# Kernel tuning notes

Measured on AMD Instinct MI355X. Metric: run time of the kernel, lower is better.

Reference implementation:

```python
import jax, jax.numpy as jnp
import numpy as np

B, T, DI, D = 8, 256, 64, 128
PRED_LEN, OUT_DIM = 96, 7
LN_EPS = 1e-5


def setup_inputs() -> dict:
    key = jax.random.key(0)
    ks = jax.random.split(key, 10)
    s = lambda k, shape, sc: (jax.random.normal(k, shape, jnp.float32) * sc)
    return {
        'x': s(ks[0], (B, T, DI), 1.0),
        'W_b': s(ks[1], (DI, D), DI ** -0.5), 'b_b': jnp.zeros((D,), jnp.float32),
        'Wk': s(ks[2], (D, D), D ** -0.5),
        'Wv': s(ks[3], (D, D), D ** -0.5),
        'Wq': s(ks[4], (D, D), D ** -0.5),
        'W_m': s(ks[5], (D, 3), D ** -0.5), 'b_m': jnp.zeros((3,), jnp.float32),
        'W_f': s(ks[6], (2 * D, D), (2 * D) ** -0.5), 'b_f': jnp.zeros((D,), jnp.float32),
        'W1': s(ks[7], (D, D), D ** -0.5), 'b1': jnp.zeros((D,), jnp.float32),
        'g1': jnp.ones((D,), jnp.float32), 'be1': jnp.zeros((D,), jnp.float32),
        'W2': s(ks[8], (D, PRED_LEN * OUT_DIM), D ** -0.5),
        'b2': jnp.zeros((PRED_LEN * OUT_DIM,), jnp.float32),
    }


def _layernorm(h, g, b):
    mu = h.mean(-1, keepdims=True)
    var = jnp.mean((h - mu) ** 2, -1, keepdims=True)
    return (h - mu) * jax.lax.rsqrt(var + LN_EPS) * g + b


def _forward(x, W_b, b_b, Wk, Wv, Wq, W_m, b_m, W_f, b_f, W1, b1, g1, be1, W2, b2):
    # Backbone P: feature extraction -> f_t  [B,T,D]
    f = jax.nn.gelu(x @ W_b + b_b)
    # Meta-learner: per-step (theta_t, eta_t, alpha_t)
    meta = jax.nn.sigmoid(f @ W_m + b_m)               # [B,T,3]
    theta = 0.01 * meta[..., 0]                         # learning rate
    eta = meta[..., 1]                                  # momentum
    alpha = 0.1 * meta[..., 2]                          # forget/decay
    # Key/value/query projections (precomputed; recurrence is in M,S only)
    k = f @ Wk; v = f @ Wv; q = f @ Wq                  # [B,T,D] each
    seq = (jnp.swapaxes(k, 0, 1), jnp.swapaxes(v, 0, 1), jnp.swapaxes(q, 0, 1),
           theta.T, eta.T, alpha.T)                     # time-major
    M0 = jnp.zeros((B, D, D), f.dtype)
    S0 = jnp.zeros((B, D, D), f.dtype)

    def step(carry, inp):
        M, S = carry
        kt, vt, qt, th, et, al = inp
        # grad of 0.5*||M k - v||^2 wrt M  (rank-1 outer product)
        err = jnp.einsum('bij,bj->bi', M, kt) - vt
        grad = jnp.einsum('bi,bj->bij', err, kt)
        S = et[:, None, None] * S - th[:, None, None] * grad
        M = (1.0 - al)[:, None, None] * M + S
        m_t = jnp.einsum('bij,bj->bi', M, qt)           # retrieve
        return (M, S), m_t

    (_, _), m_seq = jax.lax.scan(step, (M0, S0), seq)
    m = jnp.swapaxes(m_seq, 0, 1)                       # [B,T,D]
    # Gated fusion
    gate = jax.nn.sigmoid(jnp.concatenate([f, m], -1) @ W_f + b_f)
    fused = f * gate + m * (1.0 - gate)
    # Prediction head on last timestep (dropout=0 / eval)
    last = fused[:, -1, :]
    h = jax.nn.gelu(_layernorm(last @ W1 + b1, g1, be1))
    out = h @ W2 + b2
    return out.reshape(B, PRED_LEN, OUT_DIM)


def reference(x, W_b, b_b, Wk, Wv, Wq, W_m, b_m, W_f, b_f, W1, b1, g1, be1, W2, b2):
    return _forward(x, W_b, b_b, Wk, Wv, Wq, W_m, b_m, W_f, b_f, W1, b1, g1, be1, W2, b2)
```

## Files before the change

### kernel.cpp

```cpp
#include <hip/hip_runtime.h>
#include <hip/hip_bf16.h>

#define BB 8
#define TT 256
#define DIN 64
#define DD 128

__device__ __forceinline__ float gelu_tanh(float x) {
  float x3 = x * x * x;
  return 0.5f * x * (1.0f + tanhf(0.7978845608028654f * (x + 0.044715f * x3)));
}
__device__ __forceinline__ float sigmoidf(float x) {
  return 1.0f / (1.0f + __expf(-x));
}

template <typename T> __device__ __forceinline__ float getv(const void* p, int i);
template <> __device__ __forceinline__ float getv<float>(const void* p, int i) {
  return ((const float*)p)[i];
}
template <> __device__ __forceinline__ float getv<__hip_bfloat16>(const void* p, int i) {
  return __bfloat162float(((const __hip_bfloat16*)p)[i]);
}

template <int CTRL>
__device__ __forceinline__ float dpp_add(float x) {
  int s = __builtin_amdgcn_update_dpp(0, __float_as_int(x), CTRL, 0xF, 0xF, true);
  return x + __int_as_float(s);
}

__device__ __forceinline__ float rowsum16(float p) {
  p = dpp_add<0xB1>(p);
  p = dpp_add<0x4E>(p);
  p = dpp_add<0x124>(p);
  p = dpp_add<0x128>(p);
  return p;
}

__device__ __forceinline__ void gload_lds16(const void* g, void* l) {
  __builtin_amdgcn_global_load_lds(
      (const __attribute__((address_space(1))) void*)g,
      (__attribute__((address_space(3))) void*)l, 16, 0, 0);
}

__global__ void k0_detect(const void* x, int* flag) {
  __shared__ int cnt;
  if (threadIdx.x == 0) cnt = 0;
  __syncthreads();
  const unsigned short* u = (const unsigned short*)x;
  int good = 0;
  for (int idx = threadIdx.x; idx < 2048; idx += 256) {
    unsigned int bits = ((unsigned int)u[idx]) << 16;
    float f = __uint_as_float(bits);
    float a = fabsf(f);
    if (a == 0.0f || (a > 1e-4f && a < 100.0f)) good++;
  }
  atomicAdd(&cnt, good);
  __syncthreads();
  if (threadIdx.x == 0) *flag = (cnt >= 1536) ? 1 : 0;
}

template <typename T>
__device__ void k1_body(const void* x, const void* W_b, const void* b_b,
                        const void* Wk, const void* Wv, const void* Wq,
                        const void* W_m, const void* b_m,
                        float* kout, float* vout, float* scal4,
                        float* q_last, float* f_last) {
  const int row = blockIdx.x;
  const int b = row >> 8, t = row & 255;
  const int tid = threadIdx.x;
  __shared__ float xs[DIN];
  __shared__ float fs[DD];
  if (tid < DIN) xs[tid] = getv<T>(x, row * DIN + tid);
  __syncthreads();

  float acc = getv<T>(b_b, tid);
#pragma unroll 8
  for (int d = 0; d < DIN; ++d) acc += xs[d] * getv<T>(W_b, d * DD + tid);
  float f = gelu_tanh(acc);
  fs[tid] = f;
  __syncthreads();

  float ak = 0.0f, av = 0.0f;
#pragma unroll 8
  for (int c = 0; c < DD; ++c) {
    float fc = fs[c];
    ak += fc * getv<T>(Wk, c * DD + tid);
    av += fc * getv<T>(Wv, c * DD + tid);
  }
  kout[row * DD + tid] = ak;
  vout[row * DD + tid] = av;

  if (t == TT - 1) {
    float aq = 0.0f;
#pragma unroll 8
    for (int c = 0; c < DD; ++c) aq += fs[c] * getv<T>(Wq, c * DD + tid);
    q_last[b * DD + tid] = aq;
    f_last[b * DD + tid] = f;
  }
  if (tid < 4) {
    float val = 0.0f;
    if (tid < 3) {
      float a = getv<T>(b_m, tid);
      for (int c = 0; c < DD; ++c) a += fs[c] * getv<T>(W_m, c * 3 + tid);
      float s = sigmoidf(a);
      val = (tid == 0) ? 0.01f * s : ((tid == 1) ? s : 0.1f * s);
    }
    scal4[row * 4 + tid] = val;
  }
}

__global__ __launch_bounds__(128) void k1_kern(
    const void* x, const void* W_b, const void* b_b, const void* Wk,
    const void* Wv, const void* Wq, const void* W_m, const void* b_m,
    const int* flag, float* kout, float* vout, float* scal4, float* q_last,
    float* f_last) {
  if (*flag)
    k1_body<__hip_bfloat16>(x, W_b, b_b, Wk, Wv, Wq, W_m, b_m, kout, vout,
                            scal4, q_last, f_last);
  else
    k1_body<float>(x, W_b, b_b, Wk, Wv, Wq, W_m, b_m, kout, vout, scal4,
                   q_last, f_last);
}

__global__ __launch_bounds__(64) void k2_scan(
    const float* __restrict__ kbuf, const float* __restrict__ vbuf,
    const float* __restrict__ scal, const float* __restrict__ q_last,
    float* __restrict__ m_last) {
  const int tid = threadIdx.x;
  const int g = tid & 15;
  const int cidx = tid >> 4;
  const int chain = blockIdx.x * 4 + cidx;
  const int b = chain >> 7;
  const int i = chain & 127;
  const int i0 = (blockIdx.x * 4) & 127;

  __shared__ float kl[2][32 * DD];
  __shared__ float vl[TT * 4];
  __shared__ float4 scl[TT];

  const float* kslice = kbuf + (size_t)b * TT * DD;
  const float* vslice = vbuf + (size_t)b * TT * DD;

  for (int idx = tid; idx < TT * 4; idx += 64)
    vl[idx] = vslice[(idx >> 2) * DD + i0 + (idx & 3)];
  const float4* sp4 = (const float4*)scal + b * TT;
  for (int idx = tid; idx < TT; idx += 64) scl[idx] = sp4[idx];

#define K2_GLL(CH, BUF)                                                      \
  {                                                                          \
    const float* gs = kslice + (CH) * 32 * DD + tid * 4;                     \
    _Pragma("unroll") for (int j = 0; j < 16; ++j)                           \
        gload_lds16(gs + j * 256, &kl[BUF][j * 256]);                        \
  }
  K2_GLL(0, 0);

  float4 Ma = {0, 0, 0, 0}, Mb = {0, 0, 0, 0};
  float4 Sa = {0, 0, 0, 0}, Sb = {0, 0, 0, 0};

#define K2_STEP(KA, KB, VV, SC)                                              \
  {                                                                          \
    float p = (Ma.x * KA.x + Ma.y * KA.y) + (Ma.z * KA.z + Ma.w * KA.w) +    \
              (Mb.x * KB.x + Mb.y * KB.y) + (Mb.z * KB.z + Mb.w * KB.w);     \
    p = rowsum16(p);                                                         \
    const float err = p - VV;                                                \
    const float c = SC.x * err;                             \
    const float et = SC.y;                                          \
    const float am = 1.0f - SC.z;                             \
    Sa.x = et * Sa.x - c * KA.x;  Ma.x = am * Ma.x + Sa.x;                   \
    Sa.y = et * Sa.y - c * KA.y;  Ma.y = am * Ma.y + Sa.y;                   \
    Sa.z = et * Sa.z - c * KA.z;  Ma.z = am * Ma.z + Sa.z;                   \
    Sa.w = et * Sa.w - c * KA.w;  Ma.w = am * Ma.w + Sa.w;                   \
    Sb.x = et * Sb.x - c * KB.x;  Mb.x = am * Mb.x + Sb.x;                   \
    Sb.y = et * Sb.y - c * KB.y;  Mb.y = am * Mb.y + Sb.y;                   \
    Sb.z = et * Sb.z - c * KB.z;  Mb.z = am * Mb.z + Sb.z;                   \
    Sb.w = et * Sb.w - c * KB.w;  Mb.w = am * Mb.w + Sb.w;                   \
  }

  for (int ch = 0; ch < 8; ++ch) {
    asm volatile("s_waitcnt vmcnt(0) lgkmcnt(0)" ::: "memory");
    if (ch < 7) K2_GLL(ch + 1, (ch + 1) & 1);

    const float* kc = &kl[ch & 1][0];
    const int tbase = ch * 32;

    float4 ka = *(const float4*)(kc + g * 8);
    float4 kb = *(const float4*)(kc + g * 8 + 4);
    float vv = vl[tbase * 4 + cidx];
    float4 sc = scl[tbase];

#pragma unroll
    for (int tt = 0; tt < 32; ++tt) {
      float4 nka, nkb, nsc;
      float nv;
      if (tt < 31) {
        nka = *(const float4*)(kc + (tt + 1) * DD + g * 8);
        nkb = *(const float4*)(kc + (tt + 1) * DD + g * 8 + 4);
        nv = vl[(tbase + tt + 1) * 4 + cidx];
        nsc = scl[tbase + tt + 1];
      }
      K2_STEP(ka, kb, vv, sc);
      if (tt < 31) { ka = nka; kb = nkb; vv = nv; sc = nsc; }
    }
  }
#undef K2_STEP
#undef K2_GLL

  const float4* qp = (const float4*)(q_last + b * DD) + (g << 1);
  float4 qa = qp[0], qb = qp[1];
  float p = (Ma.x * qa.x + Ma.y * qa.y) + (Ma.z * qa.z + Ma.w * qa.w) +
            (Mb.x * qb.x + Mb.y * qb.y) + (Mb.z * qb.z + Mb.w * qb.w);
  p = rowsum16(p);
  if (g == 0) m_last[b * DD + i] = p;
}

template <typename T>
__device__ void k3_body(const float* f_last, const float* m_last,
                        const void* W_f, const void* b_f, const void* W1,
                        const void* b1, const void* g1, const void* be1,
                        const void* W2, const void* b2, void* out) {
  const int b = blockIdx.x, tid = threadIdx.x;
  __shared__ float fm[2 * DD];
  __shared__ float fused[DD];
  __shared__ float tmp[DD];
  __shared__ float h[DD];
  __shared__ float smu, srs;

  fm[tid] = (tid < DD) ? f_last[b * DD + tid] : m_last[b * DD + tid - DD];
  __syncthreads();

  if (tid < DD) {
    float a = getv<T>(b_f, tid);
#pragma unroll 8
    for (int c = 0; c < 2 * DD; ++c) a += fm[c] * getv<T>(W_f, c * DD + tid);
    float gte = sigmoidf(a);
    fused[tid] = fm[tid] * gte + fm[DD + tid] * (1.0f - gte);
  }
  __syncthreads();

  if (tid < DD) {
    float a = getv<T>(b1, tid);
#pragma unroll 8
    for (int c = 0; c < DD; ++c) a += fused[c] * getv<T>(W1, c * DD + tid);
    tmp[tid] = a;
  }
  __syncthreads();

  if (tid == 0) {
    float s = 0.0f;
    for (int c = 0; c < DD; ++c) s += tmp[c];
    float mu = s / (float)DD;
    float s2 = 0.0f;
    for (int c = 0; c < DD; ++c) {
      float d = tmp[c] - mu;
      s2 += d * d;
    }
    smu = mu;
    srs = rsqrtf(s2 / (float)DD + 1e-5f);
  }
  __syncthreads();

  if (tid < DD)
    h[tid] = gelu_tanh((tmp[tid] - smu) * srs * getv<T>(g1, tid) +
                       getv<T>(be1, tid));
  __syncthreads();

  for (int j = tid; j < 672; j += 256) {
    float a = getv<T>(b2, j);
#pragma unroll 8
    for (int c = 0; c < DD; ++c) a += h[c] * getv<T>(W2, c * 672 + j);
    if (sizeof(T) == 2)
      ((__hip_bfloat16*)out)[b * 672 + j] = __float2bfloat16(a);
    else
      ((float*)out)[b * 672 + j] = a;
  }
}

__global__ __launch_bounds__(256) void k3_kern(
    const float* f_last, const float* m_last, const void* W_f,
    const void* b_f, const void* W1, const void* b1, const void* g1,
    const void* be1, const void* W2, const void* b2, const int* flag,
    void* out) {
  if (*flag)
    k3_body<__hip_bfloat16>(f_last, m_last, W_f, b_f, W1, b1, g1, be1, W2, b2,
                            out);
  else
    k3_body<float>(f_last, m_last, W_f, b_f, W1, b1, g1, be1, W2, b2, out);
}

extern "C" void kernel_launch(void* const* d_in, const int* in_sizes, int n_in,
                              void* d_out, int out_size, void* d_ws,
                              size_t ws_size, hipStream_t stream) {
  const void* x   = d_in[0];
  const void* W_b = d_in[1];
  const void* b_b = d_in[2];
  const void* Wk  = d_in[3];
  const void* Wv  = d_in[4];
  const void* Wq  = d_in[5];
  const void* W_m = d_in[6];
  const void* b_m = d_in[7];
  const void* W_f = d_in[8];
  const void* b_f = d_in[9];
  const void* W1  = d_in[10];
  const void* b1  = d_in[11];
  const void* g1  = d_in[12];
  const void* be1 = d_in[13];
  const void* W2  = d_in[14];
  const void* b2  = d_in[15];

  float* w = (float*)d_ws;
  float* kbuf   = w;
  float* vbuf   = w + 262144;
  float* scal4  = w + 524288;
  float* q_last = w + 532480;
  float* f_last = w + 533504;
  float* m_last = w + 534528;
  int*   flag   = (int*)(w + 535552);

  k0_detect<<<1, 256, 0, stream>>>(x, flag);
  k1_kern<<<BB * TT, 128, 0, stream>>>(x, W_b, b_b, Wk, Wv, Wq, W_m, b_m,
                                       flag, kbuf, vbuf, scal4, q_last,
                                       f_last);
  k2_scan<<<256, 64, 0, stream>>>(kbuf, vbuf, scal4, q_last, m_last);
  k3_kern<<<BB, 256, 0, stream>>>(f_last, m_last, W_f, b_f, W1, b1, g1, be1,
                                  W2, b2, flag, d_out);
}
```

Measured before the change: 179.0 us.

## Split prediction head into two kernels with split-K parallel matvecs

The single 8-block head kernel is split in two. The first kernel uses 1024-thread blocks whose partial sums split the reduction dimension of the gate and W1 matvecs, and it computes LayerNorm statistics with wavefront shuffles instead of a serial loop in one thread. The second kernel spreads the W2 output matvec over 88 blocks, also splitting the reduction dimension. The aim is to shorten the serial tail after the scan, at the cost of one extra launch and a round-trip through global memory. Variance is now computed as E[x²]−μ², which is slightly less numerically robust.

```diff
diff --git a/kernel.cpp b/kernel.cpp
--- a/kernel.cpp
+++ b/kernel.cpp
@@ -214,77 +214,132 @@
 }
 
 template <typename T>
-__device__ void k3_body(const float* f_last, const float* m_last,
-                        const void* W_f, const void* b_f, const void* W1,
-                        const void* b1, const void* g1, const void* be1,
-                        const void* W2, const void* b2, void* out) {
+__device__ void k3a_body(const float* f_last, const float* m_last,
+                         const void* W_f, const void* b_f, const void* W1,
+                         const void* b1, const void* g1, const void* be1,
+                         float* h_buf) {
   const int b = blockIdx.x, tid = threadIdx.x;
+  const int o = tid & 127, s = tid >> 7;
   __shared__ float fm[2 * DD];
+  __shared__ float part[1024];
   __shared__ float fused[DD];
   __shared__ float tmp[DD];
-  __shared__ float h[DD];
   __shared__ float smu, srs;
 
-  fm[tid] = (tid < DD) ? f_last[b * DD + tid] : m_last[b * DD + tid - DD];
-  __syncthreads();
-
+  if (tid < 2 * DD)
+    fm[tid] = (tid < DD) ? f_last[b * DD + tid] : m_last[b * DD + tid - DD];
+  __syncthreads();
+
+  {
+    float a = 0.0f;
+#pragma unroll 8
+    for (int cc = 0; cc < 32; ++cc) {
+      const int c = s * 32 + cc;
+      a += fm[c] * getv<T>(W_f, c * DD + o);
+    }
+    part[tid] = a;
+  }
+  __syncthreads();
   if (tid < DD) {
     float a = getv<T>(b_f, tid);
-#pragma unroll 8
-    for (int c = 0; c < 2 * DD; ++c) a += fm[c] * getv<T>(W_f, c * DD + tid);
+#pragma unroll
+    for (int ss = 0; ss < 8; ++ss) a += part[ss * DD + tid];
     float gte = sigmoidf(a);
     fused[tid] = fm[tid] * gte + fm[DD + tid] * (1.0f - gte);
   }
   __syncthreads();
 
+  {
+    float a = 0.0f;
+#pragma unroll
+    for (int cc = 0; cc < 16; ++cc) {
+      const int c = s * 16 + cc;
+      a += fused[c] * getv<T>(W1, c * DD + o);
+    }
+    part[tid] = a;
+  }
+  __syncthreads();
   if (tid < DD) {
     float a = getv<T>(b1, tid);
-#pragma unroll 8
-    for (int c = 0; c < DD; ++c) a += fused[c] * getv<T>(W1, c * DD + tid);
+#pragma unroll
+    for (int ss = 0; ss < 8; ++ss) a += part[ss * DD + tid];
     tmp[tid] = a;
   }
   __syncthreads();
 
-  if (tid == 0) {
-    float s = 0.0f;
-    for (int c = 0; c < DD; ++c) s += tmp[c];
-    float mu = s / (float)DD;
-    float s2 = 0.0f;
-    for (int c = 0; c < DD; ++c) {
-      float d = tmp[c] - mu;
-      s2 += d * d;
-    }
-    smu = mu;
-    srs = rsqrtf(s2 / (float)DD + 1e-5f);
+  if (tid < 64) {
+    float x0 = tmp[tid], x1 = tmp[tid + 64];
+    float sm = x0 + x1;
+    float sq = x0 * x0 + x1 * x1;
+    sm = rowsum16(sm);
+    sq = rowsum16(sq);
+    sm += __shfl_xor(sm, 16); sq += __shfl_xor(sq, 16);
+    sm += __shfl_xor(sm, 32); sq += __shfl_xor(sq, 32);
+    if (tid == 0) {
+      float mu = sm / (float)DD;
+      smu = mu;
+      srs = rsqrtf(sq / (float)DD - mu * mu + 1e-5f);
+    }
   }
   __syncthreads();
 
   if (tid < DD)
-    h[tid] = gelu_tanh((tmp[tid] - smu) * srs * getv<T>(g1, tid) +
-                       getv<T>(be1, tid));
-  __syncthreads();
-
-  for (int j = tid; j < 672; j += 256) {
-    float a = getv<T>(b2, j);
-#pragma unroll 8
-    for (int c = 0; c < DD; ++c) a += h[c] * getv<T>(W2, c * 672 + j);
-    if (sizeof(T) == 2)
-      ((__hip_bfloat16*)out)[b * 672 + j] = __float2bfloat16(a);
-    else
-      ((float*)out)[b * 672 + j] = a;
-  }
-}
-
-__global__ __launch_bounds__(256) void k3_kern(
+    h_buf[b * DD + tid] = gelu_tanh((tmp[tid] - smu) * srs * getv<T>(g1, tid) +
+                                    getv<T>(be1, tid));
+}
+
+__global__ __launch_bounds__(1024) void k3a_kern(
     const float* f_last, const float* m_last, const void* W_f,
     const void* b_f, const void* W1, const void* b1, const void* g1,
-    const void* be1, const void* W2, const void* b2, const int* flag,
+    const void* be1, const int* flag, float* h_buf) {
+  if (*flag)
+    k3a_body<__hip_bfloat16>(f_last, m_last, W_f, b_f, W1, b1, g1, be1, h_buf);
+  else
+    k3a_body<float>(f_last, m_last, W_f, b_f, W1, b1, g1, be1, h_buf);
+}
+
+template <typename T>
+__device__ void k3b_body(const float* h_buf, const void* W2, const void* b2,
+                         void* out) {
+  const int b = blockIdx.x / 11;
+  const int jc = blockIdx.x % 11;
+  const int tid = threadIdx.x;
+  const int j = jc * 64 + (tid & 63);
+  const int s = tid >> 6;
+  __shared__ float hs[DD];
+  __shared__ float part[256];
+
+  if (tid < DD) hs[tid] = h_buf[b * DD + tid];
+  __syncthreads();
+
+  float a = 0.0f;
+  if (j < 672) {
+#pragma unroll 8
+    for (int cc = 0; cc < 32; ++cc) {
+      const int c = s * 32 + cc;
+      a += hs[c] * getv<T>(W2, c * 672 + j);
+    }
+  }
+  part[tid] = a;
+  __syncthreads();
+
+  if (tid < 64 && j < 672) {
+    float r = part[tid] + part[tid + 64] + part[tid + 128] + part[tid + 192] +
+              getv<T>(b2, j);
+    if (sizeof(T) == 2)
+      ((__hip_bfloat16*)out)[b * 672 + j] = __float2bfloat16(r);
+    else
+      ((float*)out)[b * 672 + j] = r;
+  }
+}
+
+__global__ __launch_bounds__(256) void k3b_kern(
+    const float* h_buf, const void* W2, const void* b2, const int* flag,
     void* out) {
   if (*flag)
-    k3_body<__hip_bfloat16>(f_last, m_last, W_f, b_f, W1, b1, g1, be1, W2, b2,
-                            out);
+    k3b_body<__hip_bfloat16>(h_buf, W2, b2, out);
   else
-    k3_body<float>(f_last, m_last, W_f, b_f, W1, b1, g1, be1, W2, b2, out);
+    k3b_body<float>(h_buf, W2, b2, out);
 }
 
 extern "C" void kernel_launch(void* const* d_in, const int* in_sizes, int n_in,
@@ -315,12 +370,14 @@
   float* f_last = w + 533504;
   float* m_last = w + 534528;
   int*   flag   = (int*)(w + 535552);
+  float* h_buf  = w + 535556;
 
   k0_detect<<<1, 256, 0, stream>>>(x, flag);
   k1_kern<<<BB * TT, 128, 0, stream>>>(x, W_b, b_b, Wk, Wv, Wq, W_m, b_m,
                                        flag, kbuf, vbuf, scal4, q_last,
                                        f_last);
   k2_scan<<<256, 64, 0, stream>>>(kbuf, vbuf, scal4, q_last, m_last);
-  k3_kern<<<BB, 256, 0, stream>>>(f_last, m_last, W_f, b_f, W1, b1, g1, be1,
-                                  W2, b2, flag, d_out);
-}
+  k3a_kern<<<BB, 1024, 0, stream>>>(f_last, m_last, W_f, b_f, W1, b1, g1,
+                                    be1, flag, h_buf);
+  k3b_kern<<<88, 256, 0, stream>>>(h_buf, W2, b2, flag, d_out);
+}
```

After: 154.4 us. 13.7% less time.
